# Kernel optimization log

Hardware: AMD Instinct MI355X
Metric: run time of the kernel (lower is better)

## Reference

```python
import jax, jax.numpy as jnp
import numpy as np

N_NODES = 50000
N_EDGES = 800000


def setup_inputs() -> dict:
    key = jax.random.key(0)
    k1, k2, k3, k4 = jax.random.split(key, 4)
    x = jax.random.normal(k1, (N_NODES, 128), dtype=jnp.float32)
    edge_index = jax.random.randint(k2, (2, N_EDGES), 0, N_NODES, dtype=jnp.int64)
    W1 = jax.random.normal(k3, (128, 64), dtype=jnp.float32) / np.sqrt(128.0)
    b1 = jnp.zeros((64,), dtype=jnp.float32)
    W2 = jax.random.normal(k4, (64, 40), dtype=jnp.float32) / np.sqrt(64.0)
    b2 = jnp.zeros((40,), dtype=jnp.float32)
    return {"x": x, "edge_index": edge_index, "W1": W1, "b1": b1, "W2": W2, "b2": b2}


def _gcn_norm(edge_index, n_nodes):
    # Add self-loops, then compute symmetric normalization D^{-1/2} A D^{-1/2}
    loop = jnp.arange(n_nodes, dtype=edge_index.dtype)
    row = jnp.concatenate([edge_index[0], loop])  # source
    col = jnp.concatenate([edge_index[1], loop])  # target
    ones = jnp.ones(row.shape[0], dtype=jnp.float32)
    deg = jax.ops.segment_sum(ones, col, num_segments=n_nodes)
    dinv = jnp.where(deg > 0, jax.lax.rsqrt(deg), 0.0)
    norm = dinv[row] * dinv[col]  # [E + N]
    return row, col, norm


def _gcn_conv(h, W, b, row, col, norm, n_nodes):
    hw = h @ W                         # transform first (smaller messages)
    msg = hw[row] * norm[:, None]      # gather + scale per edge
    agg = jax.ops.segment_sum(msg, col, num_segments=n_nodes)
    return agg + b


def reference(x, edge_index, W1, b1, W2, b2):
    n = x.shape[0]
    row, col, norm = _gcn_norm(edge_index, n)
    h = _gcn_conv(x, W1, b1, row, col, norm, n)
    h = jax.nn.relu(h)
    h = _gcn_conv(h, W2, b2, row, col, norm, n)
    return jax.nn.softmax(h, axis=-1)
```

## Files before the change

### kernel.cpp

```cpp
#include <hip/hip_runtime.h>
#include <hip/hip_fp16.h>

#define N_NODES 50000
#define N_EDGES 800000
#define F_IN   128
#define F_MID  64
#define F_OUT  40

#define SLICE_SHIFT 8
#define SLICE_SZ    256
#define NSLICE      196
#define PCHUNKS     256
#define PCHUNK_E    ((N_EDGES + PCHUNKS - 1) / PCHUNKS)
#define NCOUNT      (NSLICE * PCHUNKS)


__global__ __launch_bounds__(256) void bucket_count(const int* __restrict__ ei,
                                                    int* __restrict__ counts) {
    __shared__ int cnt[NSLICE];
    if (threadIdx.x < NSLICE) cnt[threadIdx.x] = 0;
    __syncthreads();
    int e0 = blockIdx.x * PCHUNK_E;
    int e1 = e0 + PCHUNK_E; if (e1 > N_EDGES) e1 = N_EDGES;
    for (int e = e0 + threadIdx.x; e < e1; e += 256) {
        int c = ei[N_EDGES + e];
        atomicAdd(&cnt[c >> SLICE_SHIFT], 1);
    }
    __syncthreads();
    if (threadIdx.x < NSLICE) counts[threadIdx.x * PCHUNKS + blockIdx.x] = cnt[threadIdx.x];
}


__global__ __launch_bounds__(256) void sc_bsum(const int* __restrict__ counts, int* __restrict__ bsum) {
    int idx = blockIdx.x * 256 + threadIdx.x;
    int v = (idx < NCOUNT) ? counts[idx] : 0;
#pragma unroll
    for (int off = 32; off > 0; off >>= 1) v += __shfl_xor(v, off, 64);
    __shared__ int ws[4];
    if ((threadIdx.x & 63) == 0) ws[threadIdx.x >> 6] = v;
    __syncthreads();
    if (threadIdx.x == 0) bsum[blockIdx.x] = ws[0] + ws[1] + ws[2] + ws[3];
}

__global__ __launch_bounds__(256) void sc_bscan(const int* __restrict__ bsum, int* __restrict__ boff) {
    int tid = threadIdx.x;
    int lane = tid & 63, wv = tid >> 6;
    int v = (tid < NSLICE) ? bsum[tid] : 0;
    int inc = v;
#pragma unroll
    for (int s = 1; s < 64; s <<= 1) {
        int t = __shfl_up(inc, s, 64);
        if (lane >= s) inc += t;
    }
    __shared__ int ws[4];
    if (lane == 63) ws[wv] = inc;
    __syncthreads();
    int woff = 0;
    for (int w = 0; w < wv; ++w) woff += ws[w];
    if (tid < NSLICE) boff[tid] = woff + inc - v;
}

__global__ __launch_bounds__(256) void sc_bscan2(const int* __restrict__ counts,
                                                 const int* __restrict__ boff,
                                                 int* __restrict__ choff) {
    int idx = blockIdx.x * 256 + threadIdx.x;
    int lane = threadIdx.x & 63, wv = threadIdx.x >> 6;
    int v = (idx < NCOUNT) ? counts[idx] : 0;
    int inc = v;
#pragma unroll
    for (int s = 1; s < 64; s <<= 1) {
        int t = __shfl_up(inc, s, 64);
        if (lane >= s) inc += t;
    }
    __shared__ int ws[4];
    if (lane == 63) ws[wv] = inc;
    __syncthreads();
    int off = boff[blockIdx.x];
    for (int w = 0; w < wv; ++w) off += ws[w];
    if (idx < NCOUNT) choff[idx] = off + inc - v;
}


__global__ __launch_bounds__(256) void bucket_scatter(const int* __restrict__ ei,
                                                      const int* __restrict__ choff,
                                                      int* __restrict__ pairs) {
    __shared__ int cur[NSLICE];
    if (threadIdx.x < NSLICE) cur[threadIdx.x] = choff[threadIdx.x * PCHUNKS + blockIdx.x];
    __syncthreads();
    int e0 = blockIdx.x * PCHUNK_E;
    int e1 = e0 + PCHUNK_E; if (e1 > N_EDGES) e1 = N_EDGES;
    for (int e = e0 + threadIdx.x; e < e1; e += 256) {
        int r = ei[e];
        int c = ei[N_EDGES + e];
        int pos = atomicAdd(&cur[c >> SLICE_SHIFT], 1);
        pairs[pos] = r | ((c & (SLICE_SZ - 1)) << 16);
    }
}


__global__ __launch_bounds__(256) void slice_csr(const int* __restrict__ pairs,
                                                 const int* __restrict__ choff,
                                                 int* __restrict__ rowptr,
                                                 float* __restrict__ dinv,
                                                 int* __restrict__ srcs) {
    __shared__ int hist[SLICE_SZ];
    __shared__ int wpart[4];
    int s = blockIdx.x;
    int base = choff[s * PCHUNKS];
    int end  = (s == NSLICE - 1) ? N_EDGES : choff[(s + 1) * PCHUNKS];
    int tid = threadIdx.x;
    hist[tid] = 0;
    __syncthreads();
    for (int i = base + tid; i < end; i += 256)
        atomicAdd(&hist[pairs[i] >> 16], 1);
    __syncthreads();
    int v = hist[tid];
    int lane = tid & 63, wv = tid >> 6;
    int inc = v;
#pragma unroll
    for (int st = 1; st < 64; st <<= 1) {
        int t = __shfl_up(inc, st, 64);
        if (lane >= st) inc += t;
    }
    if (lane == 63) wpart[wv] = inc;
    __syncthreads();
    int woff = 0;
    for (int w = 0; w < wv; ++w) woff += wpart[w];
    int ex = woff + inc - v;
    __syncthreads();
    hist[tid] = ex;
    int node = s * SLICE_SZ + tid;
    if (node < N_NODES) {
        rowptr[node] = base + ex;
        dinv[node]   = rsqrtf((float)v + 1.0f);
    }
    if (node == N_NODES - 1) rowptr[N_NODES] = N_EDGES;
    __syncthreads();
    for (int i = base + tid; i < end; i += 256) {
        int p = pairs[i];
        int pos = atomicAdd(&hist[p >> 16], 1);
        srcs[base + pos] = p & 0xFFFF;
    }
}


__global__ __launch_bounds__(256) void gemm1_kernel(const float* __restrict__ x,
                                                    const float* __restrict__ W1,
                                                    const float* __restrict__ dinv,
                                                    __half* __restrict__ hw1h) {
    __shared__ float sW[F_IN * F_MID];
    __shared__ float sX[64][68];
    int tid = threadIdx.x;
    const float4* W4 = (const float4*)W1;
    float4* sW4 = (float4*)sW;
    for (int i = tid; i < F_IN * F_MID / 4; i += 256) sW4[i] = W4[i];

    int row0 = blockIdx.x * 64;
    int tx = tid & 15, ty = tid >> 4;
    int c0 = tx * 4, r0 = ty * 4;
    float acc[4][4] = {};

    for (int p = 0; p < 2; ++p) {
        __syncthreads();
#pragma unroll
        for (int it = 0; it < 4; ++it) {
            int i = (tid + it * 256) * 4;
            int r = i >> 6, k = i & 63;
            float4 v = make_float4(0.f, 0.f, 0.f, 0.f);
            if (row0 + r < N_NODES)
                v = *(const float4*)&x[(size_t)(row0 + r) * F_IN + p * 64 + k];
            *(float4*)&sX[r][k] = v;
        }
        __syncthreads();
        const float* sWp = sW + p * 64 * F_MID;
#pragma unroll 4
        for (int k = 0; k < 64; ++k) {
            float4 w = *(const float4*)&sWp[k * F_MID + c0];
            float a0 = sX[r0 + 0][k];
            float a1 = sX[r0 + 1][k];
            float a2 = sX[r0 + 2][k];
            float a3 = sX[r0 + 3][k];
            acc[0][0] = fmaf(a0, w.x, acc[0][0]); acc[0][1] = fmaf(a0, w.y, acc[0][1]);
            acc[0][2] = fmaf(a0, w.z, acc[0][2]); acc[0][3] = fmaf(a0, w.w, acc[0][3]);
            acc[1][0] = fmaf(a1, w.x, acc[1][0]); acc[1][1] = fmaf(a1, w.y, acc[1][1]);
            acc[1][2] = fmaf(a1, w.z, acc[1][2]); acc[1][3] = fmaf(a1, w.w, acc[1][3]);
            acc[2][0] = fmaf(a2, w.x, acc[2][0]); acc[2][1] = fmaf(a2, w.y, acc[2][1]);
            acc[2][2] = fmaf(a2, w.z, acc[2][2]); acc[2][3] = fmaf(a2, w.w, acc[2][3]);
            acc[3][0] = fmaf(a3, w.x, acc[3][0]); acc[3][1] = fmaf(a3, w.y, acc[3][1]);
            acc[3][2] = fmaf(a3, w.z, acc[3][2]); acc[3][3] = fmaf(a3, w.w, acc[3][3]);
        }
    }
#pragma unroll
    for (int j = 0; j < 4; ++j) {
        int row = row0 + r0 + j;
        if (row < N_NODES) {
            float d = dinv[row];
            __half2 p0 = __floats2half2_rn(acc[j][0] * d, acc[j][1] * d);
            __half2 p1 = __floats2half2_rn(acc[j][2] * d, acc[j][3] * d);
            uint2 u = make_uint2(*reinterpret_cast<unsigned int*>(&p0),
                                 *reinterpret_cast<unsigned int*>(&p1));
            *reinterpret_cast<uint2*>(&hw1h[(size_t)row * F_MID + c0]) = u;
        }
    }
}


__global__ __launch_bounds__(256) void gather1_kernel(const int* __restrict__ rowptr,
                                                      const int* __restrict__ srcs,
                                                      const __half* __restrict__ hw1h,
                                                      const float* __restrict__ dinv,
                                                      const float* __restrict__ b1,
                                                      float* __restrict__ h) {
    int n = blockIdx.x * 4 + (threadIdx.x >> 6);
    int lane = threadIdx.x & 63;
    if (n >= N_NODES) return;
    int s = __builtin_amdgcn_readfirstlane(rowptr[n]);
    int e = __builtin_amdgcn_readfirstlane(rowptr[n + 1]);
    const __half* hb = hw1h + lane;
    float acc = 0.f;
    int j = s;
    for (; j + 8 <= e; j += 8) {
        int i0 = srcs[j + 0], i1 = srcs[j + 1], i2 = srcs[j + 2], i3 = srcs[j + 3];
        int i4 = srcs[j + 4], i5 = srcs[j + 5], i6 = srcs[j + 6], i7 = srcs[j + 7];
        float v0 = __half2float(hb[(size_t)i0 << 6]);
        float v1 = __half2float(hb[(size_t)i1 << 6]);
        float v2 = __half2float(hb[(size_t)i2 << 6]);
        float v3 = __half2float(hb[(size_t)i3 << 6]);
        float v4 = __half2float(hb[(size_t)i4 << 6]);
        float v5 = __half2float(hb[(size_t)i5 << 6]);
        float v6 = __half2float(hb[(size_t)i6 << 6]);
        float v7 = __half2float(hb[(size_t)i7 << 6]);
        acc += ((v0 + v1) + (v2 + v3)) + ((v4 + v5) + (v6 + v7));
    }
    for (; j + 2 <= e; j += 2) {
        int i0 = srcs[j], i1 = srcs[j + 1];
        acc += __half2float(hb[(size_t)i0 << 6]) + __half2float(hb[(size_t)i1 << 6]);
    }
    if (j < e) acc += __half2float(hb[(size_t)srcs[j] << 6]);
    float d = dinv[n];
    float v = fmaf(d, acc + __half2float(hb[(size_t)n << 6]), b1[lane]);
    h[(size_t)n * F_MID + lane] = fmaxf(v, 0.f);
}


__global__ __launch_bounds__(256) void gemm2_kernel(const float* __restrict__ h,
                                                    const float* __restrict__ W2,
                                                    const float* __restrict__ dinv,
                                                    __half* __restrict__ hw2h) {
    __shared__ float sW[F_MID * F_OUT];
    for (int i = threadIdx.x; i < F_MID * F_OUT; i += 256) sW[i] = W2[i];
    __syncthreads();
    int idx = blockIdx.x * 256 + threadIdx.x;
    int r = idx >> 6;
    int c = idx & 63;
    float acc = 0.f;
    if (c < F_OUT) {
        const float* hr = h + (size_t)r * F_MID;
#pragma unroll
        for (int k = 0; k < F_MID; ++k) acc = fmaf(hr[k], sW[k * F_OUT + c], acc);
        acc *= dinv[r];
    }
    hw2h[idx] = __float2half(acc);
}


__global__ __launch_bounds__(256) void gather2_softmax_kernel(const int* __restrict__ rowptr,
                                                              const int* __restrict__ srcs,
                                                              const __half* __restrict__ hw2h,
                                                              const float* __restrict__ dinv,
                                                              const float* __restrict__ b2,
                                                              float* __restrict__ out) {
    int n = blockIdx.x * 4 + (threadIdx.x >> 6);
    int lane = threadIdx.x & 63;
    if (n >= N_NODES) return;
    int s = __builtin_amdgcn_readfirstlane(rowptr[n]);
    int e = __builtin_amdgcn_readfirstlane(rowptr[n + 1]);
    const __half* gb = hw2h + lane;
    float acc = 0.f;
    int j = s;
    for (; j + 8 <= e; j += 8) {
        int i0 = srcs[j + 0], i1 = srcs[j + 1], i2 = srcs[j + 2], i3 = srcs[j + 3];
        int i4 = srcs[j + 4], i5 = srcs[j + 5], i6 = srcs[j + 6], i7 = srcs[j + 7];
        float v0 = __half2float(gb[(size_t)i0 << 6]);
        float v1 = __half2float(gb[(size_t)i1 << 6]);
        float v2 = __half2float(gb[(size_t)i2 << 6]);
        float v3 = __half2float(gb[(size_t)i3 << 6]);
        float v4 = __half2float(gb[(size_t)i4 << 6]);
        float v5 = __half2float(gb[(size_t)i5 << 6]);
        float v6 = __half2float(gb[(size_t)i6 << 6]);
        float v7 = __half2float(gb[(size_t)i7 << 6]);
        acc += ((v0 + v1) + (v2 + v3)) + ((v4 + v5) + (v6 + v7));
    }
    for (; j + 2 <= e; j += 2) {
        int i0 = srcs[j], i1 = srcs[j + 1];
        acc += __half2float(gb[(size_t)i0 << 6]) + __half2float(gb[(size_t)i1 << 6]);
    }
    if (j < e) acc += __half2float(gb[(size_t)srcs[j] << 6]);
    float d = dinv[n];
    float v = -3.402823466e38f;
    if (lane < F_OUT)
        v = fmaf(d, acc + __half2float(gb[(size_t)n << 6]), b2[lane]);
    float m = v;
#pragma unroll
    for (int off = 32; off > 0; off >>= 1) m = fmaxf(m, __shfl_xor(m, off, 64));
    float p = (lane < F_OUT) ? __expf(v - m) : 0.f;
    float su = p;
#pragma unroll
    for (int off = 32; off > 0; off >>= 1) su += __shfl_xor(su, off, 64);
    if (lane < F_OUT) out[(size_t)n * F_OUT + lane] = p / su;
}


extern "C" void kernel_launch(void* const* d_in, const int* in_sizes, int n_in,
                              void* d_out, int out_size, void* d_ws, size_t ws_size,
                              hipStream_t stream) {
    const float* x  = (const float*)d_in[0];
    const int*   ei = (const int*)d_in[1];
    const float* W1 = (const float*)d_in[2];
    const float* b1 = (const float*)d_in[3];
    const float* W2 = (const float*)d_in[4];
    const float* b2 = (const float*)d_in[5];
    float* out = (float*)d_out;

    char* ws = (char*)d_ws;
    size_t off = 0;
    auto alloc = [&](size_t bytes) -> void* {
        void* p = ws + off;
        off += (bytes + 255) & ~(size_t)255;
        return p;
    };
    int*    counts = (int*)   alloc(NCOUNT * sizeof(int));
    int*    bsum   = (int*)   alloc(NSLICE * sizeof(int));
    int*    boff   = (int*)   alloc(NSLICE * sizeof(int));
    int*    choff  = (int*)   alloc(NCOUNT * sizeof(int));
    int*    pairs  = (int*)   alloc((size_t)N_EDGES * sizeof(int));
    int*    rowptr = (int*)   alloc((N_NODES + 1) * sizeof(int));
    float*  dinv   = (float*) alloc(N_NODES * sizeof(float));
    int*    srcs   = (int*)   alloc((size_t)N_EDGES * sizeof(int));
    __half* hw1h   = (__half*)alloc((size_t)N_NODES * F_MID * sizeof(__half));
    float*  h      = (float*) alloc((size_t)N_NODES * F_MID * sizeof(float));
    __half* hw2h   = (__half*)alloc((size_t)N_NODES * F_MID * sizeof(__half));

    bucket_count  <<<PCHUNKS, 256, 0, stream>>>(ei, counts);
    sc_bsum       <<<(NCOUNT + 255) / 256, 256, 0, stream>>>(counts, bsum);
    sc_bscan      <<<1, 256, 0, stream>>>(bsum, boff);
    sc_bscan2     <<<(NCOUNT + 255) / 256, 256, 0, stream>>>(counts, boff, choff);
    bucket_scatter<<<PCHUNKS, 256, 0, stream>>>(ei, choff, pairs);
    slice_csr     <<<NSLICE, 256, 0, stream>>>(pairs, choff, rowptr, dinv, srcs);
    gemm1_kernel  <<<(N_NODES + 63) / 64, 256, 0, stream>>>(x, W1, dinv, hw1h);
    gather1_kernel<<<(N_NODES + 3) / 4, 256, 0, stream>>>(rowptr, srcs, hw1h, dinv, b1, h);
    gemm2_kernel  <<<(N_NODES * F_MID) / 256, 256, 0, stream>>>(h, W2, dinv, hw2h);
    gather2_softmax_kernel<<<(N_NODES + 3) / 4, 256, 0, stream>>>(rowptr, srcs, hw2h, dinv, b2, out);
}
```

Baseline: 212.6 us.

## Fuse bucket-offset scan kernels and deepen gather unrolling to 16 edges

Folds the per-slice bucket sums into bucket_count through global atomics and merges the three scan kernels into one, so each block redundantly scans the slice totals and then its own row of chunk counts. A memset takes the place of two of the launches. The gather loops in both layers now issue 16 independent half loads per iteration instead of 8, with a 4-wide and a scalar tail, to keep more memory requests in flight. The fused scan assumes PCHUNKS equals the block size of 256, and the deeper unroll may raise register pressure.

```diff
diff --git a/kernel.cpp b/kernel.cpp
--- a/kernel.cpp
+++ b/kernel.cpp
@@ -16,7 +16,8 @@
 
 
 __global__ __launch_bounds__(256) void bucket_count(const int* __restrict__ ei,
-                                                    int* __restrict__ counts) {
+                                                    int* __restrict__ counts,
+                                                    int* __restrict__ bsum) {
     __shared__ int cnt[NSLICE];
     if (threadIdx.x < NSLICE) cnt[threadIdx.x] = 0;
     __syncthreads();
@@ -27,57 +28,49 @@
         atomicAdd(&cnt[c >> SLICE_SHIFT], 1);
     }
     __syncthreads();
-    if (threadIdx.x < NSLICE) counts[threadIdx.x * PCHUNKS + blockIdx.x] = cnt[threadIdx.x];
-}
-
-
-__global__ __launch_bounds__(256) void sc_bsum(const int* __restrict__ counts, int* __restrict__ bsum) {
-    int idx = blockIdx.x * 256 + threadIdx.x;
-    int v = (idx < NCOUNT) ? counts[idx] : 0;
-#pragma unroll
-    for (int off = 32; off > 0; off >>= 1) v += __shfl_xor(v, off, 64);
+    if (threadIdx.x < NSLICE) {
+        int v = cnt[threadIdx.x];
+        counts[threadIdx.x * PCHUNKS + blockIdx.x] = v;
+        if (v) atomicAdd(&bsum[threadIdx.x], v);
+    }
+}
+
+
+__global__ __launch_bounds__(256) void sc_scan(const int* __restrict__ counts,
+                                               const int* __restrict__ bsum,
+                                               int* __restrict__ choff) {
     __shared__ int ws[4];
-    if ((threadIdx.x & 63) == 0) ws[threadIdx.x >> 6] = v;
-    __syncthreads();
-    if (threadIdx.x == 0) bsum[blockIdx.x] = ws[0] + ws[1] + ws[2] + ws[3];
-}
-
-__global__ __launch_bounds__(256) void sc_bscan(const int* __restrict__ bsum, int* __restrict__ boff) {
-    int tid = threadIdx.x;
+    __shared__ int sb[256];
+    int tid = threadIdx.x, b = blockIdx.x;
     int lane = tid & 63, wv = tid >> 6;
+
     int v = (tid < NSLICE) ? bsum[tid] : 0;
     int inc = v;
 #pragma unroll
-    for (int s = 1; s < 64; s <<= 1) {
-        int t = __shfl_up(inc, s, 64);
-        if (lane >= s) inc += t;
-    }
-    __shared__ int ws[4];
+    for (int st = 1; st < 64; st <<= 1) {
+        int t = __shfl_up(inc, st, 64);
+        if (lane >= st) inc += t;
+    }
     if (lane == 63) ws[wv] = inc;
     __syncthreads();
     int woff = 0;
     for (int w = 0; w < wv; ++w) woff += ws[w];
-    if (tid < NSLICE) boff[tid] = woff + inc - v;
-}
-
-__global__ __launch_bounds__(256) void sc_bscan2(const int* __restrict__ counts,
-                                                 const int* __restrict__ boff,
-                                                 int* __restrict__ choff) {
-    int idx = blockIdx.x * 256 + threadIdx.x;
-    int lane = threadIdx.x & 63, wv = threadIdx.x >> 6;
-    int v = (idx < NCOUNT) ? counts[idx] : 0;
-    int inc = v;
-#pragma unroll
-    for (int s = 1; s < 64; s <<= 1) {
-        int t = __shfl_up(inc, s, 64);
-        if (lane >= s) inc += t;
-    }
-    __shared__ int ws[4];
+    sb[tid] = woff + inc - v;
+    __syncthreads();
+    int boffb = sb[b];
+
+    int c = counts[b * PCHUNKS + tid];
+    inc = c;
+#pragma unroll
+    for (int st = 1; st < 64; st <<= 1) {
+        int t = __shfl_up(inc, st, 64);
+        if (lane >= st) inc += t;
+    }
     if (lane == 63) ws[wv] = inc;
     __syncthreads();
-    int off = boff[blockIdx.x];
-    for (int w = 0; w < wv; ++w) off += ws[w];
-    if (idx < NCOUNT) choff[idx] = off + inc - v;
+    woff = 0;
+    for (int w = 0; w < wv; ++w) woff += ws[w];
+    choff[b * PCHUNKS + tid] = boffb + woff + inc - c;
 }
 
 
@@ -219,9 +212,11 @@
     const __half* hb = hw1h + lane;
     float acc = 0.f;
     int j = s;
-    for (; j + 8 <= e; j += 8) {
-        int i0 = srcs[j + 0], i1 = srcs[j + 1], i2 = srcs[j + 2], i3 = srcs[j + 3];
-        int i4 = srcs[j + 4], i5 = srcs[j + 5], i6 = srcs[j + 6], i7 = srcs[j + 7];
+    for (; j + 16 <= e; j += 16) {
+        int i0 = srcs[j + 0],  i1 = srcs[j + 1],  i2 = srcs[j + 2],  i3 = srcs[j + 3];
+        int i4 = srcs[j + 4],  i5 = srcs[j + 5],  i6 = srcs[j + 6],  i7 = srcs[j + 7];
+        int i8 = srcs[j + 8],  i9 = srcs[j + 9],  iA = srcs[j + 10], iB = srcs[j + 11];
+        int iC = srcs[j + 12], iD = srcs[j + 13], iE = srcs[j + 14], iF = srcs[j + 15];
         float v0 = __half2float(hb[(size_t)i0 << 6]);
         float v1 = __half2float(hb[(size_t)i1 << 6]);
         float v2 = __half2float(hb[(size_t)i2 << 6]);
@@ -230,13 +225,26 @@
         float v5 = __half2float(hb[(size_t)i5 << 6]);
         float v6 = __half2float(hb[(size_t)i6 << 6]);
         float v7 = __half2float(hb[(size_t)i7 << 6]);
-        acc += ((v0 + v1) + (v2 + v3)) + ((v4 + v5) + (v6 + v7));
-    }
-    for (; j + 2 <= e; j += 2) {
-        int i0 = srcs[j], i1 = srcs[j + 1];
-        acc += __half2float(hb[(size_t)i0 << 6]) + __half2float(hb[(size_t)i1 << 6]);
-    }
-    if (j < e) acc += __half2float(hb[(size_t)srcs[j] << 6]);
+        float v8 = __half2float(hb[(size_t)i8 << 6]);
+        float v9 = __half2float(hb[(size_t)i9 << 6]);
+        float vA = __half2float(hb[(size_t)iA << 6]);
+        float vB = __half2float(hb[(size_t)iB << 6]);
+        float vC = __half2float(hb[(size_t)iC << 6]);
+        float vD = __half2float(hb[(size_t)iD << 6]);
+        float vE = __half2float(hb[(size_t)iE << 6]);
+        float vF = __half2float(hb[(size_t)iF << 6]);
+        acc += (((v0 + v1) + (v2 + v3)) + ((v4 + v5) + (v6 + v7)))
+             + (((v8 + v9) + (vA + vB)) + ((vC + vD) + (vE + vF)));
+    }
+    for (; j + 4 <= e; j += 4) {
+        int i0 = srcs[j], i1 = srcs[j + 1], i2 = srcs[j + 2], i3 = srcs[j + 3];
+        float v0 = __half2float(hb[(size_t)i0 << 6]);
+        float v1 = __half2float(hb[(size_t)i1 << 6]);
+        float v2 = __half2float(hb[(size_t)i2 << 6]);
+        float v3 = __half2float(hb[(size_t)i3 << 6]);
+        acc += (v0 + v1) + (v2 + v3);
+    }
+    for (; j < e; ++j) acc += __half2float(hb[(size_t)srcs[j] << 6]);
     float d = dinv[n];
     float v = fmaf(d, acc + __half2float(hb[(size_t)n << 6]), b1[lane]);
     h[(size_t)n * F_MID + lane] = fmaxf(v, 0.f);
@@ -278,9 +286,11 @@
     const __half* gb = hw2h + lane;
     float acc = 0.f;
     int j = s;
-    for (; j + 8 <= e; j += 8) {
-        int i0 = srcs[j + 0], i1 = srcs[j + 1], i2 = srcs[j + 2], i3 = srcs[j + 3];
-        int i4 = srcs[j + 4], i5 = srcs[j + 5], i6 = srcs[j + 6], i7 = srcs[j + 7];
+    for (; j + 16 <= e; j += 16) {
+        int i0 = srcs[j + 0],  i1 = srcs[j + 1],  i2 = srcs[j + 2],  i3 = srcs[j + 3];
+        int i4 = srcs[j + 4],  i5 = srcs[j + 5],  i6 = srcs[j + 6],  i7 = srcs[j + 7];
+        int i8 = srcs[j + 8],  i9 = srcs[j + 9],  iA = srcs[j + 10], iB = srcs[j + 11];
+        int iC = srcs[j + 12], iD = srcs[j + 13], iE = srcs[j + 14], iF = srcs[j + 15];
         float v0 = __half2float(gb[(size_t)i0 << 6]);
         float v1 = __half2float(gb[(size_t)i1 << 6]);
         float v2 = __half2float(gb[(size_t)i2 << 6]);
@@ -289,13 +299,26 @@
         float v5 = __half2float(gb[(size_t)i5 << 6]);
         float v6 = __half2float(gb[(size_t)i6 << 6]);
         float v7 = __half2float(gb[(size_t)i7 << 6]);
-        acc += ((v0 + v1) + (v2 + v3)) + ((v4 + v5) + (v6 + v7));
-    }
-    for (; j + 2 <= e; j += 2) {
-        int i0 = srcs[j], i1 = srcs[j + 1];
-        acc += __half2float(gb[(size_t)i0 << 6]) + __half2float(gb[(size_t)i1 << 6]);
-    }
-    if (j < e) acc += __half2float(gb[(size_t)srcs[j] << 6]);
+        float v8 = __half2float(gb[(size_t)i8 << 6]);
+        float v9 = __half2float(gb[(size_t)i9 << 6]);
+        float vA = __half2float(gb[(size_t)iA << 6]);
+        float vB = __half2float(gb[(size_t)iB << 6]);
+        float vC = __half2float(gb[(size_t)iC << 6]);
+        float vD = __half2float(gb[(size_t)iD << 6]);
+        float vE = __half2float(gb[(size_t)iE << 6]);
+        float vF = __half2float(gb[(size_t)iF << 6]);
+        acc += (((v0 + v1) + (v2 + v3)) + ((v4 + v5) + (v6 + v7)))
+             + (((v8 + v9) + (vA + vB)) + ((vC + vD) + (vE + vF)));
+    }
+    for (; j + 4 <= e; j += 4) {
+        int i0 = srcs[j], i1 = srcs[j + 1], i2 = srcs[j + 2], i3 = srcs[j + 3];
+        float v0 = __half2float(gb[(size_t)i0 << 6]);
+        float v1 = __half2float(gb[(size_t)i1 << 6]);
+        float v2 = __half2float(gb[(size_t)i2 << 6]);
+        float v3 = __half2float(gb[(size_t)i3 << 6]);
+        acc += (v0 + v1) + (v2 + v3);
+    }
+    for (; j < e; ++j) acc += __half2float(gb[(size_t)srcs[j] << 6]);
     float d = dinv[n];
     float v = -3.402823466e38f;
     if (lane < F_OUT)
@@ -331,7 +354,6 @@
     };
     int*    counts = (int*)   alloc(NCOUNT * sizeof(int));
     int*    bsum   = (int*)   alloc(NSLICE * sizeof(int));
-    int*    boff   = (int*)   alloc(NSLICE * sizeof(int));
     int*    choff  = (int*)   alloc(NCOUNT * sizeof(int));
     int*    pairs  = (int*)   alloc((size_t)N_EDGES * sizeof(int));
     int*    rowptr = (int*)   alloc((N_NODES + 1) * sizeof(int));
@@ -341,10 +363,9 @@
     float*  h      = (float*) alloc((size_t)N_NODES * F_MID * sizeof(float));
     __half* hw2h   = (__half*)alloc((size_t)N_NODES * F_MID * sizeof(__half));
 
-    bucket_count  <<<PCHUNKS, 256, 0, stream>>>(ei, counts);
-    sc_bsum       <<<(NCOUNT + 255) / 256, 256, 0, stream>>>(counts, bsum);
-    sc_bscan      <<<1, 256, 0, stream>>>(bsum, boff);
-    sc_bscan2     <<<(NCOUNT + 255) / 256, 256, 0, stream>>>(counts, boff, choff);
+    hipMemsetAsync(bsum, 0, NSLICE * sizeof(int), stream);
+    bucket_count  <<<PCHUNKS, 256, 0, stream>>>(ei, counts, bsum);
+    sc_scan       <<<NSLICE, 256, 0, stream>>>(counts, bsum, choff);
     bucket_scatter<<<PCHUNKS, 256, 0, stream>>>(ei, choff, pairs);
     slice_csr     <<<NSLICE, 256, 0, stream>>>(pairs, choff, rowptr, dinv, srcs);
     gemm1_kernel  <<<(N_NODES + 63) / 64, 256, 0, stream>>>(x, W1, dinv, hw1h);
```

Measured after the change: 214.9 us. About the same (+1.1%).

## Merge three-stage offset scan into one kernel and fuse gemm1 into slice CSR

Applied to the files above, without the earlier changes.

Replaces the three scan kernels with a single kernel in which every block recomputes per-slice totals and their prefix before scanning its own row of chunk counts. Fuses the first dense transform into the per-slice CSR build kernel, so each slice block also computes hw1 for its 256 nodes using dinv held in shared memory. This removes several kernel launches and the dinv reload, but gemm1 now runs on only 196 blocks with serial sub-tiles and more shared memory per block, which lowers parallelism.

```diff
diff --git a/kernel.cpp b/kernel.cpp
--- a/kernel.cpp
+++ b/kernel.cpp
@@ -31,53 +31,52 @@
 }
 
 
-__global__ __launch_bounds__(256) void sc_bsum(const int* __restrict__ counts, int* __restrict__ bsum) {
-    int idx = blockIdx.x * 256 + threadIdx.x;
-    int v = (idx < NCOUNT) ? counts[idx] : 0;
-#pragma unroll
-    for (int off = 32; off > 0; off >>= 1) v += __shfl_xor(v, off, 64);
+__global__ __launch_bounds__(256) void sc_scan(const int* __restrict__ counts,
+                                               int* __restrict__ choff) {
+    __shared__ int T[256];
+    __shared__ int P[256];
     __shared__ int ws[4];
-    if ((threadIdx.x & 63) == 0) ws[threadIdx.x >> 6] = v;
-    __syncthreads();
-    if (threadIdx.x == 0) bsum[blockIdx.x] = ws[0] + ws[1] + ws[2] + ws[3];
-}
-
-__global__ __launch_bounds__(256) void sc_bscan(const int* __restrict__ bsum, int* __restrict__ boff) {
-    int tid = threadIdx.x;
+    int tid = threadIdx.x, b = blockIdx.x;
     int lane = tid & 63, wv = tid >> 6;
-    int v = (tid < NSLICE) ? bsum[tid] : 0;
+
+    for (int r = wv; r < NSLICE; r += 4) {
+        const int* row = counts + r * PCHUNKS;
+        int ssum = row[lane] + row[lane + 64] + row[lane + 128] + row[lane + 192];
+#pragma unroll
+        for (int off = 32; off > 0; off >>= 1) ssum += __shfl_xor(ssum, off, 64);
+        if (lane == 0) T[r] = ssum;
+    }
+    if (tid >= NSLICE && tid < 256) T[tid] = 0;
+    __syncthreads();
+
+    int v = T[tid];
     int inc = v;
 #pragma unroll
-    for (int s = 1; s < 64; s <<= 1) {
-        int t = __shfl_up(inc, s, 64);
-        if (lane >= s) inc += t;
-    }
-    __shared__ int ws[4];
+    for (int st = 1; st < 64; st <<= 1) {
+        int t = __shfl_up(inc, st, 64);
+        if (lane >= st) inc += t;
+    }
     if (lane == 63) ws[wv] = inc;
     __syncthreads();
     int woff = 0;
     for (int w = 0; w < wv; ++w) woff += ws[w];
-    if (tid < NSLICE) boff[tid] = woff + inc - v;
-}
-
-__global__ __launch_bounds__(256) void sc_bscan2(const int* __restrict__ counts,
-                                                 const int* __restrict__ boff,
-                                                 int* __restrict__ choff) {
-    int idx = blockIdx.x * 256 + threadIdx.x;
-    int lane = threadIdx.x & 63, wv = threadIdx.x >> 6;
-    int v = (idx < NCOUNT) ? counts[idx] : 0;
-    int inc = v;
-#pragma unroll
-    for (int s = 1; s < 64; s <<= 1) {
-        int t = __shfl_up(inc, s, 64);
-        if (lane >= s) inc += t;
-    }
-    __shared__ int ws[4];
+    P[tid] = woff + inc - v;
+    __syncthreads();
+    int base_b = P[b];
+
+    __syncthreads();
+    int c = counts[b * PCHUNKS + tid];
+    inc = c;
+#pragma unroll
+    for (int st = 1; st < 64; st <<= 1) {
+        int t = __shfl_up(inc, st, 64);
+        if (lane >= st) inc += t;
+    }
     if (lane == 63) ws[wv] = inc;
     __syncthreads();
-    int off = boff[blockIdx.x];
-    for (int w = 0; w < wv; ++w) off += ws[w];
-    if (idx < NCOUNT) choff[idx] = off + inc - v;
+    woff = 0;
+    for (int w = 0; w < wv; ++w) woff += ws[w];
+    choff[b * PCHUNKS + tid] = base_b + woff + inc - c;
 }
 
 
@@ -98,13 +97,19 @@
 }
 
 
-__global__ __launch_bounds__(256) void slice_csr(const int* __restrict__ pairs,
-                                                 const int* __restrict__ choff,
-                                                 int* __restrict__ rowptr,
-                                                 float* __restrict__ dinv,
-                                                 int* __restrict__ srcs) {
+__global__ __launch_bounds__(256) void slice_csr_gemm1(const int* __restrict__ pairs,
+                                                       const int* __restrict__ choff,
+                                                       const float* __restrict__ x,
+                                                       const float* __restrict__ W1,
+                                                       int* __restrict__ rowptr,
+                                                       float* __restrict__ dinv,
+                                                       int* __restrict__ srcs,
+                                                       __half* __restrict__ hw1h) {
     __shared__ int hist[SLICE_SZ];
     __shared__ int wpart[4];
+    __shared__ float sdinv[SLICE_SZ];
+    __shared__ float sW[F_IN * F_MID];
+    __shared__ float sX[64][68];
     int s = blockIdx.x;
     int base = choff[s * PCHUNKS];
     int end  = (s == NSLICE - 1) ? N_EDGES : choff[(s + 1) * PCHUNKS];
@@ -129,10 +134,12 @@
     int ex = woff + inc - v;
     __syncthreads();
     hist[tid] = ex;
+    float dv = rsqrtf((float)v + 1.0f);
+    sdinv[tid] = dv;
     int node = s * SLICE_SZ + tid;
     if (node < N_NODES) {
         rowptr[node] = base + ex;
-        dinv[node]   = rsqrtf((float)v + 1.0f);
+        dinv[node]   = dv;
     }
     if (node == N_NODES - 1) rowptr[N_NODES] = N_EDGES;
     __syncthreads();
@@ -141,65 +148,59 @@
         int pos = atomicAdd(&hist[p >> 16], 1);
         srcs[base + pos] = p & 0xFFFF;
     }
-}
-
-
-__global__ __launch_bounds__(256) void gemm1_kernel(const float* __restrict__ x,
-                                                    const float* __restrict__ W1,
-                                                    const float* __restrict__ dinv,
-                                                    __half* __restrict__ hw1h) {
-    __shared__ float sW[F_IN * F_MID];
-    __shared__ float sX[64][68];
-    int tid = threadIdx.x;
+
     const float4* W4 = (const float4*)W1;
     float4* sW4 = (float4*)sW;
     for (int i = tid; i < F_IN * F_MID / 4; i += 256) sW4[i] = W4[i];
 
-    int row0 = blockIdx.x * 64;
     int tx = tid & 15, ty = tid >> 4;
     int c0 = tx * 4, r0 = ty * 4;
-    float acc[4][4] = {};
-
-    for (int p = 0; p < 2; ++p) {
-        __syncthreads();
-#pragma unroll
-        for (int it = 0; it < 4; ++it) {
-            int i = (tid + it * 256) * 4;
-            int r = i >> 6, k = i & 63;
-            float4 v = make_float4(0.f, 0.f, 0.f, 0.f);
-            if (row0 + r < N_NODES)
-                v = *(const float4*)&x[(size_t)(row0 + r) * F_IN + p * 64 + k];
-            *(float4*)&sX[r][k] = v;
+    int sBase = s * SLICE_SZ;
+
+    for (int sub = 0; sub < 4; ++sub) {
+        int row0 = sBase + sub * 64;
+        float acc[4][4] = {};
+        for (int p = 0; p < 2; ++p) {
+            __syncthreads();
+#pragma unroll
+            for (int it = 0; it < 4; ++it) {
+                int i = (tid + it * 256) * 4;
+                int r = i >> 6, k = i & 63;
+                float4 vx = make_float4(0.f, 0.f, 0.f, 0.f);
+                if (row0 + r < N_NODES)
+                    vx = *(const float4*)&x[(size_t)(row0 + r) * F_IN + p * 64 + k];
+                *(float4*)&sX[r][k] = vx;
+            }
+            __syncthreads();
+            const float* sWp = sW + p * 64 * F_MID;
+#pragma unroll 4
+            for (int k = 0; k < 64; ++k) {
+                float4 w = *(const float4*)&sWp[k * F_MID + c0];
+                float a0 = sX[r0 + 0][k];
+                float a1 = sX[r0 + 1][k];
+                float a2 = sX[r0 + 2][k];
+                float a3 = sX[r0 + 3][k];
+                acc[0][0] = fmaf(a0, w.x, acc[0][0]); acc[0][1] = fmaf(a0, w.y, acc[0][1]);
+                acc[0][2] = fmaf(a0, w.z, acc[0][2]); acc[0][3] = fmaf(a0, w.w, acc[0][3]);
+                acc[1][0] = fmaf(a1, w.x, acc[1][0]); acc[1][1] = fmaf(a1, w.y, acc[1][1]);
+                acc[1][2] = fmaf(a1, w.z, acc[1][2]); acc[1][3] = fmaf(a1, w.w, acc[1][3]);
+                acc[2][0] = fmaf(a2, w.x, acc[2][0]); acc[2][1] = fmaf(a2, w.y, acc[2][1]);
+                acc[2][2] = fmaf(a2, w.z, acc[2][2]); acc[2][3] = fmaf(a2, w.w, acc[2][3]);
+                acc[3][0] = fmaf(a3, w.x, acc[3][0]); acc[3][1] = fmaf(a3, w.y, acc[3][1]);
+                acc[3][2] = fmaf(a3, w.z, acc[3][2]); acc[3][3] = fmaf(a3, w.w, acc[3][3]);
+            }
         }
-        __syncthreads();
-        const float* sWp = sW + p * 64 * F_MID;
-#pragma unroll 4
-        for (int k = 0; k < 64; ++k) {
-            float4 w = *(const float4*)&sWp[k * F_MID + c0];
-            float a0 = sX[r0 + 0][k];
-            float a1 = sX[r0 + 1][k];
-            float a2 = sX[r0 + 2][k];
-            float a3 = sX[r0 + 3][k];
-            acc[0][0] = fmaf(a0, w.x, acc[0][0]); acc[0][1] = fmaf(a0, w.y, acc[0][1]);
-            acc[0][2] = fmaf(a0, w.z, acc[0][2]); acc[0][3] = fmaf(a0, w.w, acc[0][3]);
-            acc[1][0] = fmaf(a1, w.x, acc[1][0]); acc[1][1] = fmaf(a1, w.y, acc[1][1]);
-            acc[1][2] = fmaf(a1, w.z, acc[1][2]); acc[1][3] = fmaf(a1, w.w, acc[1][3]);
-            acc[2][0] = fmaf(a2, w.x, acc[2][0]); acc[2][1] = fmaf(a2, w.y, acc[2][1]);
-            acc[2][2] = fmaf(a2, w.z, acc[2][2]); acc[2][3] = fmaf(a2, w.w, acc[2][3]);
-            acc[3][0] = fmaf(a3, w.x, acc[3][0]); acc[3][1] = fmaf(a3, w.y, acc[3][1]);
-            acc[3][2] = fmaf(a3, w.z, acc[3][2]); acc[3][3] = fmaf(a3, w.w, acc[3][3]);
-        }
-    }
-#pragma unroll
-    for (int j = 0; j < 4; ++j) {
-        int row = row0 + r0 + j;
-        if (row < N_NODES) {
-            float d = dinv[row];
-            __half2 p0 = __floats2half2_rn(acc[j][0] * d, acc[j][1] * d);
-            __half2 p1 = __floats2half2_rn(acc[j][2] * d, acc[j][3] * d);
-            uint2 u = make_uint2(*reinterpret_cast<unsigned int*>(&p0),
-                                 *reinterpret_cast<unsigned int*>(&p1));
-            *reinterpret_cast<uint2*>(&hw1h[(size_t)row * F_MID + c0]) = u;
+#pragma unroll
+        for (int j = 0; j < 4; ++j) {
+            int row = row0 + r0 + j;
+            if (row < N_NODES) {
+                float d = sdinv[sub * 64 + r0 + j];
+                __half2 p0 = __floats2half2_rn(acc[j][0] * d, acc[j][1] * d);
+                __half2 p1 = __floats2half2_rn(acc[j][2] * d, acc[j][3] * d);
+                uint2 u = make_uint2(*reinterpret_cast<unsigned int*>(&p0),
+                                     *reinterpret_cast<unsigned int*>(&p1));
+                *reinterpret_cast<uint2*>(&hw1h[(size_t)row * F_MID + c0]) = u;
+            }
         }
     }
 }
@@ -330,8 +331,6 @@
         return p;
     };
     int*    counts = (int*)   alloc(NCOUNT * sizeof(int));
-    int*    bsum   = (int*)   alloc(NSLICE * sizeof(int));
-    int*    boff   = (int*)   alloc(NSLICE * sizeof(int));
     int*    choff  = (int*)   alloc(NCOUNT * sizeof(int));
     int*    pairs  = (int*)   alloc((size_t)N_EDGES * sizeof(int));
     int*    rowptr = (int*)   alloc((N_NODES + 1) * sizeof(int));
@@ -341,14 +340,11 @@
     float*  h      = (float*) alloc((size_t)N_NODES * F_MID * sizeof(float));
     __half* hw2h   = (__half*)alloc((size_t)N_NODES * F_MID * sizeof(__half));
 
-    bucket_count  <<<PCHUNKS, 256, 0, stream>>>(ei, counts);
-    sc_bsum       <<<(NCOUNT + 255) / 256, 256, 0, stream>>>(counts, bsum);
-    sc_bscan      <<<1, 256, 0, stream>>>(bsum, boff);
-    sc_bscan2     <<<(NCOUNT + 255) / 256, 256, 0, stream>>>(counts, boff, choff);
-    bucket_scatter<<<PCHUNKS, 256, 0, stream>>>(ei, choff, pairs);
-    slice_csr     <<<NSLICE, 256, 0, stream>>>(pairs, choff, rowptr, dinv, srcs);
-    gemm1_kernel  <<<(N_NODES + 63) / 64, 256, 0, stream>>>(x, W1, dinv, hw1h);
-    gather1_kernel<<<(N_NODES + 3) / 4, 256, 0, stream>>>(rowptr, srcs, hw1h, dinv, b1, h);
-    gemm2_kernel  <<<(N_NODES * F_MID) / 256, 256, 0, stream>>>(h, W2, dinv, hw2h);
+    bucket_count   <<<PCHUNKS, 256, 0, stream>>>(ei, counts);
+    sc_scan        <<<NSLICE, 256, 0, stream>>>(counts, choff);
+    bucket_scatter <<<PCHUNKS, 256, 0, stream>>>(ei, choff, pairs);
+    slice_csr_gemm1<<<NSLICE, 256, 0, stream>>>(pairs, choff, x, W1, rowptr, dinv, srcs, hw1h);
+    gather1_kernel <<<(N_NODES + 3) / 4, 256, 0, stream>>>(rowptr, srcs, hw1h, dinv, b1, h);
+    gemm2_kernel   <<<(N_NODES * F_MID) / 256, 256, 0, stream>>>(h, W2, dinv, hw2h);
     gather2_softmax_kernel<<<(N_NODES + 3) / 4, 256, 0, stream>>>(rowptr, srcs, hw2h, dinv, b2, out);
 }
```

New measurement: 241.6 us. 1.14x slower.
